# Kernel optimization log

Hardware: AMD Instinct MI355X
Metric: run time of the kernel (lower is better)

## Reference

```python
import jax, jax.numpy as jnp
import numpy as np

N = 50000        # nodes
R = 51           # enriched relations (25 fwd + 25 inverse + self-loop)
F_IN = 32        # feat_size
E = 32           # embed_size
C = 16           # num_classes
B = 30           # num_bases
NNZ = 2_000_000  # nonzeros in vertical adjacency


def _xavier(key, shape):
    # mimics nn.init.xavier_uniform_ with gain for relu (sqrt(2))
    fan_in, fan_out = shape[-2], shape[-1]
    a = np.sqrt(2.0) * np.sqrt(6.0 / (fan_in + fan_out))
    return jax.random.uniform(key, shape, jnp.float32, -a, a)


def setup_inputs() -> dict:
    key = jax.random.key(0)
    ks = jax.random.split(key, 8)
    # COO of vertical adjacency, shape (R*N, N)
    rows = jax.random.randint(ks[0], (NNZ,), 0, R * N)
    cols = jax.random.randint(ks[1], (NNZ,), 0, N)
    # row-normalized values: vals = 1 / row_degree  (sum_sparse with rows=True)
    deg = jax.ops.segment_sum(jnp.ones((NNZ,), jnp.float32), rows, num_segments=R * N)
    vals = (1.0 / jnp.maximum(deg, 1.0))[rows]
    features = jax.random.normal(ks[2], (N, F_IN), jnp.float32)
    comps1 = _xavier(ks[3], (R, B))
    bases1 = _xavier(ks[4], (B, F_IN, E))
    comps2 = _xavier(ks[5], (R, B))
    bases2 = _xavier(ks[6], (B, E, C))
    bias1 = jnp.zeros((E,), jnp.float32)
    bias2 = jnp.zeros((C,), jnp.float32)
    return {
        "features": features, "vals": vals,
        "comps1": comps1, "bases1": bases1, "bias1": bias1,
        "comps2": comps2, "bases2": bases2, "bias2": bias2,
        "rows": rows, "cols": cols,
    }


def _spmm(rows, cols, vals, x):
    # (R*N, N) sparse @ (N, f) dense -> (R*N, f)
    return jax.ops.segment_sum(vals[:, None] * x[cols], rows, num_segments=R * N)


def reference(features, vals, comps1, bases1, bias1, comps2, bases2, bias2, rows, cols):
    # layer 1: SpMM then basis-decomposed per-relation mixing
    h = _spmm(rows, cols, vals, features).reshape(R, N, F_IN)   # (r, n, f)
    w1 = jnp.einsum('rb,bfe->rfe', comps1, bases1)              # (r, f, e)
    h = jnp.einsum('rnf,rfe->ne', h, w1)                        # (n, e)
    h = jax.nn.relu(h + bias1)
    # layer 2
    h = _spmm(rows, cols, vals, h).reshape(R, N, E)             # (r, n, e)
    w2 = jnp.einsum('rb,bho->rho', comps2, bases2)              # (r, e, c)
    h = jnp.einsum('rho,rnh->no', w2, h)                        # (n, c)
    return h + bias2
```

## Files before the change

kernel.cpp:

```cpp
#include <hip/hip_runtime.h>

#define NNODES 50000
#define RREL 51
#define FIN 32
#define EDIM 32
#define CDIM 16
#define BB 30
#define NNZ_ 2000000
#define EPB 4096
#define NBUK 391
#define PCAP_MAX 2750128

typedef unsigned int uint32;
typedef unsigned short ushort;
typedef uint32 u32x2 __attribute__((ext_vector_type(2)));
typedef uint32 u32x4 __attribute__((ext_vector_type(4)));
typedef short bf16x8 __attribute__((ext_vector_type(8)));
typedef float f32x4 __attribute__((ext_vector_type(4)));
typedef float f32x16 __attribute__((ext_vector_type(16)));

static __device__ __forceinline__ uint32 pack_bf16x2(float a, float b) {
    uint32 ua = __builtin_bit_cast(uint32, a);
    uint32 ub = __builtin_bit_cast(uint32, b);
    ua += 0x7fffu + ((ua >> 16) & 1u);
    ub += 0x7fffu + ((ub >> 16) & 1u);
    return (ua >> 16) | (ub & 0xffff0000u);
}
static __device__ __forceinline__ ushort bf16_1(float x) {
    uint32 u = __builtin_bit_cast(uint32, x);
    u += 0x7fffu + ((u >> 16) & 1u);
    return (ushort)(u >> 16);
}

__global__ void k_weights2(const float* __restrict__ bases1, const float* __restrict__ bases2,
                           ushort* __restrict__ Wb1, ushort* __restrict__ Wb2) {
    int i = blockIdx.x * 256 + threadIdx.x;
    if (i < 960 * 32) {
        int e = i & 31, k = i >> 5;
        int b = k >> 5, f = k & 31;
        float v = bases1[b * 1024 + f * 32 + e];
        Wb1[((k >> 3) * 32 + e) * 8 + (k & 7)] = bf16_1(v);
    }
    if (i < 960 * 16) {
        int e = i & 15, k = i >> 4;
        int b = k >> 5, h = k & 31;
        float v = bases2[b * 512 + h * 16 + e];
        Wb2[((k >> 3) * 16 + e) * 8 + (k & 7)] = bf16_1(v);
    }
}

__global__ void k_tobf16(const float2* __restrict__ src, uint32* __restrict__ dst, int n2) {
    int i = blockIdx.x * 256 + threadIdx.x;
    if (i < n2) {
        float2 f = src[i];
        dst[i] = pack_bf16x2(f.x, f.y);
    }
}

__global__ __launch_bounds__(1024) void k_bukhist(const int* __restrict__ rows,
                                                  int* __restrict__ buk_cnt) {
    __shared__ int lc[NBUK];
    int t = threadIdx.x;
    if (t < NBUK) lc[t] = 0;
    __syncthreads();
    size_t k = (size_t)blockIdx.x * EPB + (size_t)t * 4;
    int rr[4];
    if (k + 4 <= NNZ_) {
        int4 rw = *(const int4*)(rows + k);
        rr[0] = rw.x; rr[1] = rw.y; rr[2] = rw.z; rr[3] = rw.w;
    } else {
#pragma unroll
        for (int j = 0; j < 4; j++) rr[j] = (k + j < NNZ_) ? rows[k + j] : -1;
    }
#pragma unroll
    for (int j = 0; j < 4; j++)
        if (rr[j] >= 0) {
            int rel = rr[j] / NNODES;
            int dst = rr[j] - rel * NNODES;
            atomicAdd(&lc[dst >> 7], 1);
        }
    __syncthreads();
    if (t < NBUK) atomicAdd(&buk_cnt[t], lc[t]);
}

__global__ void k_scan1(const int* __restrict__ buk_cnt, int* __restrict__ buk_base,
                        int* __restrict__ buk_cur) {
    if (threadIdx.x == 0) {
        int a = 0;
        for (int b = 0; b < NBUK; b++) { buk_base[b] = a; buk_cur[b] = a; a += buk_cnt[b]; }
        buk_base[NBUK] = a;
    }
}

__global__ __launch_bounds__(1024) void k_bucket2(const int* __restrict__ rows,
                                                  const int* __restrict__ cols,
                                                  const float* __restrict__ vals,
                                                  int* __restrict__ buk_cur,
                                                  u32x2* __restrict__ tok8,
                                                  float* __restrict__ sval_b) {
    __shared__ int bukc[NBUK], lb[NBUK], gb[NBUK];
    __shared__ int ssum[1024];
    __shared__ u32x2 st8[EPB];
    __shared__ float sv[EPB];
    int t = threadIdx.x;
    size_t base = (size_t)blockIdx.x * EPB;
    int total = (int)(((size_t)NNZ_ - base < (size_t)EPB) ? ((size_t)NNZ_ - base) : (size_t)EPB);
    if (t < NBUK) bukc[t] = 0;
    __syncthreads();
    size_t k = base + (size_t)t * 4;
    int bv[4]; uint32 tx[4], ty[4]; float vv[4];
    if (k + 4 <= NNZ_) {
        int4 rw = *(const int4*)(rows + k);
        int4 cw = *(const int4*)(cols + k);
        float4 vw = *(const float4*)(vals + k);
        int rr[4] = {rw.x, rw.y, rw.z, rw.w};
        int cc[4] = {cw.x, cw.y, cw.z, cw.w};
        vv[0] = vw.x; vv[1] = vw.y; vv[2] = vw.z; vv[3] = vw.w;
#pragma unroll
        for (int j = 0; j < 4; j++) {
            int rel = rr[j] / NNODES;
            int dst = rr[j] - rel * NNODES;
            bv[j] = dst >> 7;
            tx[j] = (uint32)dst | ((uint32)rel << 16);
            ty[j] = (uint32)cc[j] | ((uint32)rel << 16);
        }
    } else {
#pragma unroll
        for (int j = 0; j < 4; j++) {
            if (k + j < NNZ_) {
                int r = rows[k + j];
                int rel = r / NNODES;
                int dst = r - rel * NNODES;
                bv[j] = dst >> 7;
                tx[j] = (uint32)dst | ((uint32)rel << 16);
                ty[j] = (uint32)cols[k + j] | ((uint32)rel << 16);
                vv[j] = vals[k + j];
            } else bv[j] = -1;
        }
    }
#pragma unroll
    for (int j = 0; j < 4; j++)
        if (bv[j] >= 0) atomicAdd(&bukc[bv[j]], 1);
    __syncthreads();
    int v = (t < NBUK) ? bukc[t] : 0;
    ssum[t] = v;
    __syncthreads();
    for (int off = 1; off < 1024; off <<= 1) {
        int u = (t >= off) ? ssum[t - off] : 0;
        __syncthreads();
        ssum[t] += u;
        __syncthreads();
    }
    if (t < NBUK) { lb[t] = ssum[t] - v; gb[t] = atomicAdd(&buk_cur[t], v); }
    __syncthreads();
    if (t < NBUK) bukc[t] = 0;
    __syncthreads();
#pragma unroll
    for (int j = 0; j < 4; j++) {
        if (bv[j] >= 0) {
            int slot = lb[bv[j]] + atomicAdd(&bukc[bv[j]], 1);
            u32x2 w; w.x = tx[j]; w.y = ty[j];
            st8[slot] = w;
            sv[slot] = vv[j];
        }
    }
    __syncthreads();
    for (int s = t; s < total; s += 1024) {
        u32x2 w = st8[s];
        int bk = (int)((w.x & 0xFFFFu) >> 7);
        int pos = gb[bk] + (s - lb[bk]);
        tok8[pos] = w;
        sval_b[pos] = sv[s];
    }
}

__global__ __launch_bounds__(256) void k_rank3a(const u32x2* __restrict__ tok8,
                                                const int* __restrict__ buk_base,
                                                int* __restrict__ pbuk_cnt) {
    __shared__ int lcnt[128];
    __shared__ int tot;
    int b = blockIdx.x, t = threadIdx.x;
    if (t < 128) lcnt[t] = 0;
    if (t == 0) tot = 0;
    __syncthreads();
    int lo = buk_base[b], hi = buk_base[b + 1];
    for (int i = lo + t; i < hi; i += 256) atomicAdd(&lcnt[tok8[i].x & 127], 1);
    __syncthreads();
    if (t < 128) atomicAdd(&tot, (lcnt[t] + 15) & ~15);
    __syncthreads();
    if (t == 0) pbuk_cnt[b] = tot;
}

__global__ void k_scan2(const int* __restrict__ pbuk_cnt, int* __restrict__ pbuk_base) {
    if (threadIdx.x == 0) {
        int a = 0;
        for (int b = 0; b < NBUK; b++) { pbuk_base[b] = a; a += pbuk_cnt[b]; }
        pbuk_base[NBUK] = a;
    }
}

__global__ __launch_bounds__(256) void k_place(const u32x2* __restrict__ tok8,
                                               const float* __restrict__ sval_b,
                                               const int* __restrict__ buk_base,
                                               const int* __restrict__ pbuk_base,
                                               int* __restrict__ pdst_base,
                                               uint32* __restrict__ pe_sr,
                                               float* __restrict__ pe_val) {
    __shared__ int lcnt[128], lexc[128], lrank[128], ssc[128];
    int b = blockIdx.x, t = threadIdx.x;
    int lo = buk_base[b], hi = buk_base[b + 1], pb = pbuk_base[b];
    if (t < 128) { lcnt[t] = 0; lrank[t] = 0; }
    __syncthreads();
    for (int i = lo + t; i < hi; i += 256) atomicAdd(&lcnt[tok8[i].x & 127], 1);
    __syncthreads();
    int v = 0;
    if (t < 128) { v = (lcnt[t] + 15) & ~15; ssc[t] = v; }
    __syncthreads();
    for (int off = 1; off < 128; off <<= 1) {
        int u = (t >= off && t < 128) ? ssc[t - off] : 0;
        __syncthreads();
        if (t < 128) ssc[t] += u;
        __syncthreads();
    }
    if (t < 128) {
        lexc[t] = ssc[t] - v;
        int d = (b << 7) + t;
        if (d <= NNODES) pdst_base[d] = pb + lexc[t];
    }
    __syncthreads();
    for (int i = lo + t; i < hi; i += 256) {
        u32x2 w = tok8[i];
        int dl = (int)(w.x & 127u);
        int pos = pb + lexc[dl] + atomicAdd(&lrank[dl], 1);
        pe_sr[pos] = w.y;
        pe_val[pos] = sval_b[i];
    }
    if (t < 128) {
        int s0 = pb + lexc[t] + lcnt[t];
        int s1 = pb + lexc[t] + ((lcnt[t] + 15) & ~15);
        for (int i = s0; i < s1; i++) { pe_sr[i] = 0u; pe_val[i] = 0.f; }
    }
}

template <int FO, bool RELU, bool BF16OUT>
__global__ __launch_bounds__(256) void k_fused(const uint32* __restrict__ pe_sr,
                                               const float* __restrict__ pe_val,
                                               const int* __restrict__ pdst_base,
                                               const u32x4* __restrict__ Xb,
                                               const u32x4* __restrict__ Wb,
                                               const float* __restrict__ comps,
                                               const float* __restrict__ bias,
                                               void* __restrict__ outp) {
    __shared__ ushort comps_lb[RREL * 32];
    __shared__ uint32 eds[4][64];
    __shared__ __align__(16) ushort xst[4][4][512];
    __shared__ __align__(16) ushort ubuf[4][2][968];
    int t = threadIdx.x, lane = t & 63, wv = t >> 6;
    for (int i = t; i < RREL * 32; i += 256) {
        int r = i >> 5, b = i & 31;
        comps_lb[i] = (b < BB) ? bf16_1(comps[r * BB + b]) : (ushort)0;
    }
    __syncthreads();
    int m = lane & 31, hf = lane >> 5, k0 = hf * 8;
    int ln15 = lane & 15, quad = lane >> 4;
    int d0 = (blockIdx.x * 4 + wv) * 8;
    if (d0 >= NNODES) return;

    auto ccprep = [&](int wi) -> u32x4 {
        uint32 c[8];
#pragma unroll
        for (int j = 0; j < 8; j++) {
            uint32 sr = eds[wv][wi * 16 + k0 + j];
            c[j] = (uint32)comps_lb[((sr >> 16) << 5) | m];
        }
        u32x4 r = { c[0] | (c[1] << 16), c[2] | (c[3] << 16),
                    c[4] | (c[5] << 16), c[6] | (c[7] << 16) };
        return r;
    };
    auto scale8 = [&](u32x4 g, float vm) -> u32x4 {
        u32x4 r;
#pragma unroll
        for (int q = 0; q < 4; q++) {
            float lo = __builtin_bit_cast(float, g[q] << 16) * vm;
            float hi = __builtin_bit_cast(float, g[q] & 0xffff0000u) * vm;
            r[q] = pack_bf16x2(lo, hi);
        }
        return r;
    };
    auto dowin = [&](int wi, u32x4 avq, f32x16 a) -> f32x16 {
        const ushort* xs = &xst[wv][wi][0];
        uint32 b0 = (uint32)xs[(k0 + 0) * 32 + m] | ((uint32)xs[(k0 + 1) * 32 + m] << 16);
        uint32 b1 = (uint32)xs[(k0 + 2) * 32 + m] | ((uint32)xs[(k0 + 3) * 32 + m] << 16);
        uint32 b2 = (uint32)xs[(k0 + 4) * 32 + m] | ((uint32)xs[(k0 + 5) * 32 + m] << 16);
        uint32 b3 = (uint32)xs[(k0 + 6) * 32 + m] | ((uint32)xs[(k0 + 7) * 32 + m] << 16);
        u32x4 bvq = { b0, b1, b2, b3 };
        return __builtin_amdgcn_mfma_f32_32x32x16_bf16(
            __builtin_bit_cast(bf16x8, avq), __builtin_bit_cast(bf16x8, bvq), a, 0, 0, 0);
    };

    int base0 = pdst_base[d0];
    uint32 pvs = __builtin_nontemporal_load(&pe_sr[base0 + lane]);
    float  pvv = __builtin_nontemporal_load(&pe_val[base0 + lane]);
    u32x4 gx0, gx1, gx2, gx3;
    {
        int s0_ = __shfl((int)pvs, (lane >> 2), 64);
        gx0 = Xb[(size_t)((uint32)s0_ & 0xFFFFu) * 4 + (lane & 3)];
        int s1_ = __shfl((int)pvs, 16 + (lane >> 2), 64);
        gx1 = Xb[(size_t)((uint32)s1_ & 0xFFFFu) * 4 + (lane & 3)];
        int s2_ = __shfl((int)pvs, 32 + (lane >> 2), 64);
        gx2 = Xb[(size_t)((uint32)s2_ & 0xFFFFu) * 4 + (lane & 3)];
        int s3_ = __shfl((int)pvs, 48 + (lane >> 2), 64);
        gx3 = Xb[(size_t)((uint32)s3_ & 0xFFFFu) * 4 + (lane & 3)];
    }

#pragma unroll 1
    for (int batch = 0; batch < 4; batch++) {
        int db = d0 + batch * 2;
#pragma unroll 1
        for (int s = 0; s < 2; s++) {
            int d = db + s;
            int lo = pdst_base[d], segEnd = pdst_base[d + 1];
            f32x16 acc;
#pragma unroll
            for (int i = 0; i < 16; i++) acc[i] = 0.f;
#pragma unroll 1
            for (int c0 = lo; c0 < segEnd; c0 += 64) {
                eds[wv][lane] = pvs;
                int nxt = c0 + 64; if (nxt > segEnd) nxt = segEnd;
                uint32 npvs = __builtin_nontemporal_load(&pe_sr[nxt + lane]);
                float  npvv = __builtin_nontemporal_load(&pe_val[nxt + lane]);
                int nwin = (segEnd - c0) >> 4;
                if (nwin > 4) nwin = 4;
                u32x4 av0, av1, av2, av3;
                av0 = ccprep(0);
                if (nwin > 1) av1 = ccprep(1);
                if (nwin > 2) av2 = ccprep(2);
                if (nwin > 3) av3 = ccprep(3);
                {
                    float vm = __shfl(pvv, (lane >> 2), 64);
                    *(u32x4*)&xst[wv][0][lane * 8] = scale8(gx0, vm);
                }
                if (nwin > 1) {
                    float vm = __shfl(pvv, 16 + (lane >> 2), 64);
                    *(u32x4*)&xst[wv][1][lane * 8] = scale8(gx1, vm);
                }
                if (nwin > 2) {
                    float vm = __shfl(pvv, 32 + (lane >> 2), 64);
                    *(u32x4*)&xst[wv][2][lane * 8] = scale8(gx2, vm);
                }
                if (nwin > 3) {
                    float vm = __shfl(pvv, 48 + (lane >> 2), 64);
                    *(u32x4*)&xst[wv][3][lane * 8] = scale8(gx3, vm);
                }
                acc = dowin(0, av0, acc);
                if (nwin > 1) acc = dowin(1, av1, acc);
                if (nwin > 2) acc = dowin(2, av2, acc);
                if (nwin > 3) acc = dowin(3, av3, acc);
                {
                    int s0_ = __shfl((int)npvs, (lane >> 2), 64);
                    gx0 = Xb[(size_t)((uint32)s0_ & 0xFFFFu) * 4 + (lane & 3)];
                    int s1_ = __shfl((int)npvs, 16 + (lane >> 2), 64);
                    gx1 = Xb[(size_t)((uint32)s1_ & 0xFFFFu) * 4 + (lane & 3)];
                    int s2_ = __shfl((int)npvs, 32 + (lane >> 2), 64);
                    gx2 = Xb[(size_t)((uint32)s2_ & 0xFFFFu) * 4 + (lane & 3)];
                    int s3_ = __shfl((int)npvs, 48 + (lane >> 2), 64);
                    gx3 = Xb[(size_t)((uint32)s3_ & 0xFFFFu) * 4 + (lane & 3)];
                }
                pvs = npvs; pvv = npvv;
            }
#pragma unroll
            for (int r = 0; r < 16; r++) {
                int b = (r & 3) + 8 * (r >> 2) + 4 * hf;
                float vme = acc[r];
                float vot = __shfl_xor(vme, 1, 64);
                if (b < BB && !(m & 1)) {
                    *(uint32*)&ubuf[wv][s][b * 32 + m] = pack_bf16x2(vme, vot);
                }
            }
        }
        const int NT = FO / 16;
        f32x4 a2[NT];
#pragma unroll
        for (int tt = 0; tt < NT; tt++)
#pragma unroll
            for (int i = 0; i < 4; i++) a2[tt][i] = 0.f;
#pragma unroll 6
        for (int ks = 0; ks < 30; ks++) {
            bf16x8 af = *(const bf16x8*)&ubuf[wv][ln15 & 1][ks * 32 + quad * 8];
#pragma unroll
            for (int tt = 0; tt < NT; tt++) {
                bf16x8 bf2 = __builtin_bit_cast(bf16x8, Wb[(ks * 4 + quad) * FO + ln15 + 16 * tt]);
                a2[tt] = __builtin_amdgcn_mfma_f32_16x16x32_bf16(af, bf2, a2[tt], 0, 0, 0);
            }
        }
        if (quad == 0) {
#pragma unroll
            for (int r = 0; r < 2; r++) {
                int dst = db + r;
                if (dst < NNODES) {
                    if (BF16OUT) {
                        ushort* hp = (ushort*)outp;
#pragma unroll
                        for (int tt = 0; tt < NT; tt++) {
                            float o = a2[tt][r] + bias[ln15 + 16 * tt];
                            if (RELU) o = fmaxf(o, 0.f);
                            hp[(size_t)dst * FO + ln15 + 16 * tt] = bf16_1(o);
                        }
                    } else {
                        float o = a2[0][r] + bias[ln15];
                        if (RELU) o = fmaxf(o, 0.f);
                        ((float*)outp)[(size_t)dst * FO + ln15] = o;
                    }
                }
            }
        }
    }
}

extern "C" void kernel_launch(void* const* d_in, const int* in_sizes, int n_in,
                              void* d_out, int out_size, void* d_ws, size_t ws_size,
                              hipStream_t stream) {
    const float* features = (const float*)d_in[0];
    const float* vals     = (const float*)d_in[1];
    const float* comps1   = (const float*)d_in[2];
    const float* bases1   = (const float*)d_in[3];
    const float* bias1    = (const float*)d_in[4];
    const float* comps2   = (const float*)d_in[5];
    const float* bases2   = (const float*)d_in[6];
    const float* bias2    = (const float*)d_in[7];
    const int*   rows     = (const int*)d_in[8];
    const int*   cols     = (const int*)d_in[9];
    float* out = (float*)d_out;

    float* ws = (float*)d_ws;
    size_t o = 0;
    ushort* Wb1 = (ushort*)(ws + o); o += 960 * 32 / 2;
    ushort* Wb2 = (ushort*)(ws + o); o += 960 * 16 / 2;
    uint32* Xb  = (uint32*)(ws + o); o += (size_t)NNODES * 16;
    uint32* h1b = (uint32*)(ws + o); o += (size_t)NNODES * 16;
    uint32* pe_sr  = (uint32*)(ws + o); o += PCAP_MAX;
    float*  pe_val = (float*)(ws + o);  o += PCAP_MAX;
    int* pdst_base = (int*)(ws + o); o += NNODES + 8;
    int* buk_cnt   = (int*)(ws + o); o += NBUK;
    int* buk_base  = (int*)(ws + o); o += NBUK + 1;
    int* buk_cur   = (int*)(ws + o); o += NBUK;
    int* pbuk_cnt  = (int*)(ws + o); o += NBUK;
    int* pbuk_base = (int*)(ws + o); o += NBUK + 1;
    o = (o + 1) & ~(size_t)1;
    u32x2* tok8 = (u32x2*)(ws + o); o += 2 * (size_t)NNZ_;
    float* sval_b = (float*)(ws + o); o += (size_t)NNZ_;

    const int NB = (NNZ_ + EPB - 1) / EPB;

    hipMemsetAsync(buk_cnt, 0, NBUK * sizeof(int), stream);

    k_weights2<<<(960 * 32 + 255) / 256, 256, 0, stream>>>(bases1, bases2, Wb1, Wb2);
    k_tobf16<<<(NNODES * FIN / 2 + 255) / 256, 256, 0, stream>>>((const float2*)features, Xb,
                                                                 NNODES * FIN / 2);
    k_bukhist<<<NB, 1024, 0, stream>>>(rows, buk_cnt);
    k_scan1<<<1, 64, 0, stream>>>(buk_cnt, buk_base, buk_cur);
    k_bucket2<<<NB, 1024, 0, stream>>>(rows, cols, vals, buk_cur, tok8, sval_b);
    k_rank3a<<<NBUK, 256, 0, stream>>>(tok8, buk_base, pbuk_cnt);
    k_scan2<<<1, 64, 0, stream>>>(pbuk_cnt, pbuk_base);
    k_place<<<NBUK, 256, 0, stream>>>(tok8, sval_b, buk_base, pbuk_base, pdst_base, pe_sr, pe_val);

    k_fused<EDIM, true, true><<<(NNODES + 31) / 32, 256, 0, stream>>>(
        pe_sr, pe_val, pdst_base, (const u32x4*)Xb, (const u32x4*)Wb1, comps1, bias1, h1b);
    k_fused<CDIM, false, false><<<(NNODES + 31) / 32, 256, 0, stream>>>(
        pe_sr, pe_val, pdst_base, (const u32x4*)h1b, (const u32x4*)Wb2, comps2, bias2, out);
}
```

Before: 381.4 us.

## Deepen gather prefetch pipeline and batch four destinations per output MFMA

Edge-index loads now run two chunks ahead and the feature gathers one chunk ahead, issued before the current chunk's MFMAs rather than after, to hide gather latency. Empty destination segments are padded to 16 entries so the lookahead can always cross segment boundaries. The second-stage mixing MFMA now covers four destinations per batch instead of two, filling more of the 16-row tile. This costs extra registers, more shared memory for ubuf, and padding work for empty segments.

```diff
diff --git a/kernel.cpp b/kernel.cpp
--- a/kernel.cpp
+++ b/kernel.cpp
@@ -9,7 +9,7 @@
 #define NNZ_ 2000000
 #define EPB 4096
 #define NBUK 391
-#define PCAP_MAX 2750128
+#define PCAP_MAX 2800128
 
 typedef unsigned int uint32;
 typedef unsigned short ushort;
@@ -186,7 +186,13 @@
     int lo = buk_base[b], hi = buk_base[b + 1];
     for (int i = lo + t; i < hi; i += 256) atomicAdd(&lcnt[tok8[i].x & 127], 1);
     __syncthreads();
-    if (t < 128) atomicAdd(&tot, (lcnt[t] + 15) & ~15);
+    if (t < 128) {
+        int d = (b << 7) + t;
+        int v = (lcnt[t] + 15) & ~15;
+        if (d < NNODES && v == 0) v = 16;
+        if (d >= NNODES) v = 0;
+        atomicAdd(&tot, v);
+    }
     __syncthreads();
     if (t == 0) pbuk_cnt[b] = tot;
 }
@@ -214,7 +220,13 @@
     for (int i = lo + t; i < hi; i += 256) atomicAdd(&lcnt[tok8[i].x & 127], 1);
     __syncthreads();
     int v = 0;
-    if (t < 128) { v = (lcnt[t] + 15) & ~15; ssc[t] = v; }
+    if (t < 128) {
+        int d = (b << 7) + t;
+        v = (lcnt[t] + 15) & ~15;
+        if (d < NNODES && v == 0) v = 16;
+        if (d >= NNODES) v = 0;
+        ssc[t] = v;
+    }
     __syncthreads();
     for (int off = 1; off < 128; off <<= 1) {
         int u = (t >= off && t < 128) ? ssc[t - off] : 0;
@@ -225,7 +237,7 @@
     if (t < 128) {
         lexc[t] = ssc[t] - v;
         int d = (b << 7) + t;
-        if (d <= NNODES) pdst_base[d] = pb + lexc[t];
+        if (d <= NNODES + 4) pdst_base[d] = pb + lexc[t];
     }
     __syncthreads();
     for (int i = lo + t; i < hi; i += 256) {
@@ -237,7 +249,7 @@
     }
     if (t < 128) {
         int s0 = pb + lexc[t] + lcnt[t];
-        int s1 = pb + lexc[t] + ((lcnt[t] + 15) & ~15);
+        int s1 = pb + lexc[t] + v;
         for (int i = s0; i < s1; i++) { pe_sr[i] = 0u; pe_val[i] = 0.f; }
     }
 }
@@ -254,7 +266,7 @@
     __shared__ ushort comps_lb[RREL * 32];
     __shared__ uint32 eds[4][64];
     __shared__ __align__(16) ushort xst[4][4][512];
-    __shared__ __align__(16) ushort ubuf[4][2][968];
+    __shared__ __align__(16) ushort ubuf[4][4][968];
     int t = threadIdx.x, lane = t & 63, wv = t >> 6;
     for (int i = t; i < RREL * 32; i += 256) {
         int r = i >> 5, b = i & 31;
@@ -297,38 +309,46 @@
         return __builtin_amdgcn_mfma_f32_32x32x16_bf16(
             __builtin_bit_cast(bf16x8, avq), __builtin_bit_cast(bf16x8, bvq), a, 0, 0, 0);
     };
-
-    int base0 = pdst_base[d0];
-    uint32 pvs = __builtin_nontemporal_load(&pe_sr[base0 + lane]);
-    float  pvv = __builtin_nontemporal_load(&pe_val[base0 + lane]);
-    u32x4 gx0, gx1, gx2, gx3;
-    {
-        int s0_ = __shfl((int)pvs, (lane >> 2), 64);
-        gx0 = Xb[(size_t)((uint32)s0_ & 0xFFFFu) * 4 + (lane & 3)];
-        int s1_ = __shfl((int)pvs, 16 + (lane >> 2), 64);
-        gx1 = Xb[(size_t)((uint32)s1_ & 0xFFFFu) * 4 + (lane & 3)];
-        int s2_ = __shfl((int)pvs, 32 + (lane >> 2), 64);
-        gx2 = Xb[(size_t)((uint32)s2_ & 0xFFFFu) * 4 + (lane & 3)];
-        int s3_ = __shfl((int)pvs, 48 + (lane >> 2), 64);
-        gx3 = Xb[(size_t)((uint32)s3_ & 0xFFFFu) * 4 + (lane & 3)];
-    }
+    auto gather4 = [&](uint32 ps, u32x4& g0, u32x4& g1, u32x4& g2, u32x4& g3) {
+        int s0_ = __shfl((int)ps, (lane >> 2), 64);
+        g0 = Xb[(size_t)((uint32)s0_ & 0xFFFFu) * 4 + (lane & 3)];
+        int s1_ = __shfl((int)ps, 16 + (lane >> 2), 64);
+        g1 = Xb[(size_t)((uint32)s1_ & 0xFFFFu) * 4 + (lane & 3)];
+        int s2_ = __shfl((int)ps, 32 + (lane >> 2), 64);
+        g2 = Xb[(size_t)((uint32)s2_ & 0xFFFFu) * 4 + (lane & 3)];
+        int s3_ = __shfl((int)ps, 48 + (lane >> 2), 64);
+        g3 = Xb[(size_t)((uint32)s3_ & 0xFFFFu) * 4 + (lane & 3)];
+    };
+
+    int A0 = pdst_base[d0];
+    int e1_ = pdst_base[d0 + 1];
+    int A1 = A0 + 64; if (A1 > e1_) A1 = e1_;
+    uint32 pvsC = __builtin_nontemporal_load(&pe_sr[A0 + lane]);
+    float  pvvC = __builtin_nontemporal_load(&pe_val[A0 + lane]);
+    uint32 pvsN = __builtin_nontemporal_load(&pe_sr[A1 + lane]);
+    float  pvvN = __builtin_nontemporal_load(&pe_val[A1 + lane]);
+    u32x4 gx0, gx1, gx2, gx3, gy0, gy1, gy2, gy3;
+    gather4(pvsC, gx0, gx1, gx2, gx3);
 
 #pragma unroll 1
-    for (int batch = 0; batch < 4; batch++) {
-        int db = d0 + batch * 2;
+    for (int batch = 0; batch < 2; batch++) {
+        int db = d0 + batch * 4;
 #pragma unroll 1
-        for (int s = 0; s < 2; s++) {
+        for (int s = 0; s < 4; s++) {
             int d = db + s;
-            int lo = pdst_base[d], segEnd = pdst_base[d + 1];
+            int lo = pdst_base[d], segEnd = pdst_base[d + 1], e2 = pdst_base[d + 2];
             f32x16 acc;
 #pragma unroll
             for (int i = 0; i < 16; i++) acc[i] = 0.f;
 #pragma unroll 1
             for (int c0 = lo; c0 < segEnd; c0 += 64) {
-                eds[wv][lane] = pvs;
-                int nxt = c0 + 64; if (nxt > segEnd) nxt = segEnd;
-                uint32 npvs = __builtin_nontemporal_load(&pe_sr[nxt + lane]);
-                float  npvv = __builtin_nontemporal_load(&pe_val[nxt + lane]);
+                int aN = c0 + 64; if (aN > segEnd) aN = segEnd;
+                int lim = (aN == segEnd) ? e2 : segEnd;
+                int aNN = aN + 64; if (aNN > lim) aNN = lim;
+                uint32 pvsP = __builtin_nontemporal_load(&pe_sr[aNN + lane]);
+                float  pvvP = __builtin_nontemporal_load(&pe_val[aNN + lane]);
+                gather4(pvsN, gy0, gy1, gy2, gy3);
+                eds[wv][lane] = pvsC;
                 int nwin = (segEnd - c0) >> 4;
                 if (nwin > 4) nwin = 4;
                 u32x4 av0, av1, av2, av3;
@@ -337,36 +357,27 @@
                 if (nwin > 2) av2 = ccprep(2);
                 if (nwin > 3) av3 = ccprep(3);
                 {
-                    float vm = __shfl(pvv, (lane >> 2), 64);
+                    float vm = __shfl(pvvC, (lane >> 2), 64);
                     *(u32x4*)&xst[wv][0][lane * 8] = scale8(gx0, vm);
                 }
                 if (nwin > 1) {
-                    float vm = __shfl(pvv, 16 + (lane >> 2), 64);
+                    float vm = __shfl(pvvC, 16 + (lane >> 2), 64);
                     *(u32x4*)&xst[wv][1][lane * 8] = scale8(gx1, vm);
                 }
                 if (nwin > 2) {
-                    float vm = __shfl(pvv, 32 + (lane >> 2), 64);
+                    float vm = __shfl(pvvC, 32 + (lane >> 2), 64);
                     *(u32x4*)&xst[wv][2][lane * 8] = scale8(gx2, vm);
                 }
                 if (nwin > 3) {
-                    float vm = __shfl(pvv, 48 + (lane >> 2), 64);
+                    float vm = __shfl(pvvC, 48 + (lane >> 2), 64);
                     *(u32x4*)&xst[wv][3][lane * 8] = scale8(gx3, vm);
                 }
                 acc = dowin(0, av0, acc);
                 if (nwin > 1) acc = dowin(1, av1, acc);
                 if (nwin > 2) acc = dowin(2, av2, acc);
                 if (nwin > 3) acc = dowin(3, av3, acc);
-                {
-                    int s0_ = __shfl((int)npvs, (lane >> 2), 64);
-                    gx0 = Xb[(size_t)((uint32)s0_ & 0xFFFFu) * 4 + (lane & 3)];
-                    int s1_ = __shfl((int)npvs, 16 + (lane >> 2), 64);
-                    gx1 = Xb[(size_t)((uint32)s1_ & 0xFFFFu) * 4 + (lane & 3)];
-                    int s2_ = __shfl((int)npvs, 32 + (lane >> 2), 64);
-                    gx2 = Xb[(size_t)((uint32)s2_ & 0xFFFFu) * 4 + (lane & 3)];
-                    int s3_ = __shfl((int)npvs, 48 + (lane >> 2), 64);
-                    gx3 = Xb[(size_t)((uint32)s3_ & 0xFFFFu) * 4 + (lane & 3)];
-                }
-                pvs = npvs; pvv = npvv;
+                gx0 = gy0; gx1 = gy1; gx2 = gy2; gx3 = gy3;
+                pvsC = pvsN; pvvC = pvvN; pvsN = pvsP; pvvN = pvvP;
             }
 #pragma unroll
             for (int r = 0; r < 16; r++) {
@@ -386,7 +397,7 @@
             for (int i = 0; i < 4; i++) a2[tt][i] = 0.f;
 #pragma unroll 6
         for (int ks = 0; ks < 30; ks++) {
-            bf16x8 af = *(const bf16x8*)&ubuf[wv][ln15 & 1][ks * 32 + quad * 8];
+            bf16x8 af = *(const bf16x8*)&ubuf[wv][ln15 & 3][ks * 32 + quad * 8];
 #pragma unroll
             for (int tt = 0; tt < NT; tt++) {
                 bf16x8 bf2 = __builtin_bit_cast(bf16x8, Wb[(ks * 4 + quad) * FO + ln15 + 16 * tt]);
@@ -395,7 +406,7 @@
         }
         if (quad == 0) {
 #pragma unroll
-            for (int r = 0; r < 2; r++) {
+            for (int r = 0; r < 4; r++) {
                 int dst = db + r;
                 if (dst < NNODES) {
                     if (BF16OUT) {
```

New measurement: 365.6 us. 4.1% less time.
